# Optimization experiments

Measured on AMD Instinct MI355X. Metric: run time of the kernel, lower is better.

## Reference

```python
import jax
jax.config.update("jax_enable_x64", True)
import jax.numpy as jnp
import numpy as np

SAMPLE_RATE = 44100
HOP = 512
B, N_MELS, T = 8, 128, 2048
L = T * HOP  # 1,048,576 samples


def _lerp_up(x, out_len):
    # torch F.interpolate(mode='linear', align_corners=True): [B,C,Tin]->[B,C,out_len]
    t_in = x.shape[-1]
    pos = jnp.arange(out_len, dtype=jnp.float64) * ((t_in - 1) / (out_len - 1))
    i0 = jnp.floor(pos).astype(jnp.int32)
    i1 = jnp.minimum(i0 + 1, t_in - 1)
    w = (pos - i0).astype(x.dtype)
    return x[..., i0] * (1 - w) + x[..., i1] * w


def _conv1d(x, w, b, pad):
    y = jax.lax.conv_general_dilated(x, w, (1,), [(pad, pad)],
                                     dimension_numbers=("NCH", "OIH", "NCH"))
    return y + b[None, :, None]


def setup_inputs() -> dict:
    key = jax.random.key(0)
    ks = jax.random.split(key, 9)
    mel_frames = jax.random.normal(ks[0], (B, N_MELS, T), dtype=jnp.float32)
    # realistic f0: 80..380 Hz
    f0_frames = 80.0 + 300.0 * jax.random.uniform(ks[1], (B, T), dtype=jnp.float32)
    noise = jax.random.normal(ks[2], (B, L), dtype=jnp.float32)
    w1 = jax.random.normal(ks[3], (128, N_MELS, 7), dtype=jnp.float32) * 0.05
    b1 = jnp.zeros((128,), jnp.float32)
    w2 = jax.random.normal(ks[4], (128, 128, 3), dtype=jnp.float32) * 0.05
    b2 = jnp.zeros((128,), jnp.float32)
    w3 = jax.random.normal(ks[5], (2, 128, 3), dtype=jnp.float32) * 0.05
    b3 = jnp.zeros((2,), jnp.float32)
    return {"mel_frames": mel_frames, "f0_frames": f0_frames, "noise": noise,
            "w1": w1, "b1": b1, "w2": w2, "b2": b2, "w3": w3, "b3": b3}


def reference(mel_frames, f0_frames, noise, w1, b1, w2, b2, w3, b3):
    # --- comb source ---
    f0 = _lerp_up(f0_frames[:, None, :], L)  # [B,1,L]
    phase = jnp.cumsum(f0.astype(jnp.float64) / SAMPLE_RATE, axis=-1)
    phase = phase - jnp.round(phase)
    phase = phase.astype(f0.dtype)
    combtooth = jnp.sinc(SAMPLE_RATE * phase / (f0 + 1e-8))[:, 0, :]  # [B,L]
    # --- magnitude network ---
    h = jax.nn.leaky_relu(_conv1d(mel_frames, w1, b1, 3), 0.2)
    h = jax.nn.leaky_relu(_conv1d(h, w2, b2, 1), 0.2)
    mags = jnp.clip(_conv1d(h, w3, b3, 1), 0.0, 1.0)  # [B,2,T]
    mags = _lerp_up(mags, L)  # [B,2,L]
    noise_sig = jnp.clip(noise * mags[:, 0, :], -1.0, 1.0)
    comb_sig = jnp.clip(combtooth * mags[:, 1, :], -1.0, 1.0)
    signal = jnp.clip(noise_sig + comb_sig, -1.0, 1.0)
    return (signal[:, None, :], (comb_sig[:, None, :], noise_sig[:, None, :]))
```

## Files before the change

kernel.cpp:

```cpp
#include <hip/hip_runtime.h>
#include <math.h>

#define BATCH 8
#define NMEL 128
#define TT 2048
#define LL 1048576
#define NCHUNK 128
#define CHUNK 8192

static constexpr double RATIO = 2047.0 / 1048575.0;
static constexpr double INV_SR = 1.0 / 44100.0;

__device__ __forceinline__ float f0_at(const float* __restrict__ row, int n) {
    double pos = (double)n * RATIO;
    double fp = floor(pos);
    int i0 = (int)fp;
    int i1 = i0 + 1; if (i1 > TT - 1) i1 = TT - 1;
    float w = (float)(pos - fp);
    return row[i0] * (1.0f - w) + row[i1] * w;
}

__global__ __launch_bounds__(256) void wtrans_kernel(
    const float* __restrict__ w1, const float* __restrict__ w2,
    float* __restrict__ w1t, float* __restrict__ w2t)
{
    int i = blockIdx.x * 256 + threadIdx.x;
    if (i < 896 * 128) {
        int m = i >> 7, co = i & 127;
        w1t[i] = w1[co * 896 + m];
    }
    if (i < 384 * 128) {
        int m = i >> 7, co = i & 127;
        w2t[i] = w2[co * 384 + m];
    }
}

#define XSTR 48
#define HSTR 44
__global__ __launch_bounds__(256, 2) void fused_conv(
    const float* __restrict__ mel,
    const float* __restrict__ w1t,
    const float* __restrict__ b1,
    const float* __restrict__ w2t,
    const float* __restrict__ b2,
    const float* __restrict__ w3,
    const float* __restrict__ b3,
    float* __restrict__ mags)
{
    __shared__ float Xs[NMEL * XSTR];
    __shared__ float H1[NMEL * HSTR];
    __shared__ float H2[NMEL * HSTR];
    __shared__ float red[2][4][32];

    int b  = blockIdx.x >> 6;
    int t0 = (blockIdx.x & 63) * 32;
    int tid = threadIdx.x;
    const float* melb = mel + (size_t)b * NMEL * TT;

    #pragma unroll
    for (int it = 0; it < 6; ++it) {
        int idx = tid + it * 256;
        int ci = idx / 12, q = idx - ci * 12;
        int t = t0 - 8 + q * 4;
        float4 v = make_float4(0.f, 0.f, 0.f, 0.f);
        if (t >= 0 && t + 3 < TT) v = *(const float4*)(melb + ci * TT + t);
        *(float4*)(&Xs[ci * XSTR + q * 4]) = v;
    }
    if (tid < 128) { H1[tid * HSTR + 0] = 0.f; H1[tid * HSTR + 41] = 0.f; }
    __syncthreads();

    int cog = tid >> 3;
    int tg  = tid & 7;
    int xbase = 1 + tg * 5;

    {
        float acc[4][5];
        #pragma unroll
        for (int j = 0; j < 4; ++j) {
            float bj = b1[cog * 4 + j];
            #pragma unroll
            for (int i = 0; i < 5; ++i) acc[j][i] = bj;
        }
        for (int ci = 0; ci < NMEL; ++ci) {
            float xv[11];
            #pragma unroll
            for (int i = 0; i < 11; ++i) xv[i] = Xs[ci * XSTR + xbase + i];
            const float* wr = w1t + (size_t)(ci * 7) * 128 + cog * 4;
            #pragma unroll
            for (int k = 0; k < 7; ++k) {
                float4 w4 = *(const float4*)(wr + k * 128);
                float wv[4] = {w4.x, w4.y, w4.z, w4.w};
                #pragma unroll
                for (int j = 0; j < 4; ++j)
                    #pragma unroll
                    for (int i = 0; i < 5; ++i)
                        acc[j][i] = fmaf(wv[j], xv[i + k], acc[j][i]);
            }
        }
        #pragma unroll
        for (int j = 0; j < 4; ++j)
            #pragma unroll
            for (int i = 0; i < 5; ++i) {
                int t = t0 - 4 + tg * 5 + i;
                float v = acc[j][i];
                v = v > 0.0f ? v : 0.2f * v;
                if (t < 0 || t >= TT) v = 0.0f;
                H1[(cog * 4 + j) * HSTR + 1 + tg * 5 + i] = v;
            }
    }
    __syncthreads();

    {
        float acc[4][5];
        #pragma unroll
        for (int j = 0; j < 4; ++j) {
            float bj = b2[cog * 4 + j];
            #pragma unroll
            for (int i = 0; i < 5; ++i) acc[j][i] = bj;
        }
        int hbase = tg * 5;
        for (int ci = 0; ci < NMEL; ++ci) {
            float xv[7];
            #pragma unroll
            for (int i = 0; i < 7; ++i) xv[i] = H1[ci * HSTR + hbase + i];
            const float* wr = w2t + (size_t)(ci * 3) * 128 + cog * 4;
            #pragma unroll
            for (int k = 0; k < 3; ++k) {
                float4 w4 = *(const float4*)(wr + k * 128);
                float wv[4] = {w4.x, w4.y, w4.z, w4.w};
                #pragma unroll
                for (int j = 0; j < 4; ++j)
                    #pragma unroll
                    for (int i = 0; i < 5; ++i)
                        acc[j][i] = fmaf(wv[j], xv[i + k], acc[j][i]);
            }
        }
        #pragma unroll
        for (int j = 0; j < 4; ++j)
            #pragma unroll
            for (int i = 0; i < 5; ++i) {
                int t = t0 - 4 + tg * 5 + i;
                float v = acc[j][i];
                v = v > 0.0f ? v : 0.2f * v;
                if (t < 0 || t >= TT) v = 0.0f;
                H2[(cog * 4 + j) * HSTR + tg * 5 + i] = v;
            }
    }
    __syncthreads();

    {
        int o   = tid >> 7;
        int cig = (tid >> 5) & 3;
        int tt  = tid & 31;
        float a = 0.0f;
        for (int cl = 0; cl < 32; ++cl) {
            int ci = cig * 32 + cl;
            #pragma unroll
            for (int k = 0; k < 3; ++k)
                a = fmaf(w3[o * 384 + ci * 3 + k], H2[ci * HSTR + tt + 3 + k], a);
        }
        red[o][cig][tt] = a;
    }
    __syncthreads();
    if (tid < 64) {
        int o = tid >> 5, tt = tid & 31;
        float s = b3[o] + red[o][0][tt] + red[o][1][tt] + red[o][2][tt] + red[o][3][tt];
        s = fminf(fmaxf(s, 0.0f), 1.0f);
        mags[((size_t)b * 2 + o) * TT + t0 + tt] = s;
    }
}

__global__ __launch_bounds__(256) void chunksum_kernel(
    const float* __restrict__ f0f, double* __restrict__ sums)
{
    int b = blockIdx.x >> 7;
    int c = blockIdx.x & (NCHUNK - 1);
    const float* row = f0f + b * TT;
    int tid = threadIdx.x;
    int start = c * CHUNK + tid * 32;
    double s = 0.0;
    #pragma unroll
    for (int i = 0; i < 32; ++i)
        s += (double)f0_at(row, start + i) * INV_SR;
    __shared__ double red[256];
    red[tid] = s;
    __syncthreads();
    for (int off = 128; off > 0; off >>= 1) {
        if (tid < off) red[tid] += red[tid + off];
        __syncthreads();
    }
    if (tid == 0) sums[blockIdx.x] = red[0];
}

__global__ void scanoff_kernel(const double* __restrict__ sums, double* __restrict__ offs)
{
    int b = threadIdx.x;
    if (b < BATCH) {
        double run = 0.0;
        for (int c = 0; c < NCHUNK; ++c) {
            offs[b * NCHUNK + c] = run;
            run += sums[b * NCHUNK + c];
        }
    }
}

__device__ __forceinline__ int swz(int idx) { return idx ^ ((idx >> 5) & 31); }

__global__ __launch_bounds__(256) void final_kernel(
    const float* __restrict__ f0f,
    const float* __restrict__ noise,
    const float* __restrict__ mags,
    const double* __restrict__ offs,
    float* __restrict__ out)
{
    int b = blockIdx.x >> 7;
    int c = blockIdx.x & (NCHUNK - 1);
    const float* row = f0f + b * TT;
    int tid = threadIdx.x;
    __shared__ float fracs[CHUNK];
    __shared__ double red[256];

    int chunkBase = c * CHUNK;
    int start = chunkBase + tid * 32;

    float f0v[32];
    double s = 0.0;
    #pragma unroll
    for (int i = 0; i < 32; ++i) {
        f0v[i] = f0_at(row, start + i);
        s += (double)f0v[i] * INV_SR;
    }
    red[tid] = s;
    __syncthreads();
    for (int off = 1; off < 256; off <<= 1) {
        double v = (tid >= off) ? red[tid - off] : 0.0;
        __syncthreads();
        red[tid] += v;
        __syncthreads();
    }
    double run = offs[b * NCHUNK + c] + red[tid] - s;

    #pragma unroll
    for (int i = 0; i < 32; ++i) {
        run += (double)f0v[i] * INV_SR;
        double fr = run - rint(run);
        fracs[swz(tid * 32 + i)] = (float)fr;
    }
    __syncthreads();

    const size_t BL = (size_t)BATCH * LL;
    const size_t outBase = (size_t)b * LL;
    const float* m0row = mags + (size_t)b * 2 * TT;
    const float* m1row = m0row + TT;

    #pragma unroll 4
    for (int i = 0; i < 32; ++i) {
        int idx = i * 256 + tid;
        int n = chunkBase + idx;
        double pos = (double)n * RATIO;
        double fp = floor(pos);
        int i0 = (int)fp;
        int i1 = i0 + 1; if (i1 > TT - 1) i1 = TT - 1;
        float w = (float)(pos - fp);
        float f0 = row[i0] * (1.0f - w) + row[i1] * w;
        float m0 = m0row[i0] * (1.0f - w) + m0row[i1] * w;
        float m1 = m1row[i0] * (1.0f - w) + m1row[i1] * w;
        float ph = fracs[swz(idx)];
        float x = 44100.0f * ph / (f0 + 1e-8f);
        float px = 3.14159265358979323f * x;
        float comb = (x == 0.0f) ? 1.0f : (sinf(px) / px);
        float nz = noise[outBase + n];
        float ns = fminf(fmaxf(nz * m0, -1.0f), 1.0f);
        float cs = fminf(fmaxf(comb * m1, -1.0f), 1.0f);
        float sig = fminf(fmaxf(ns + cs, -1.0f), 1.0f);
        out[outBase + n]          = sig;
        out[BL + outBase + n]     = cs;
        out[2 * BL + outBase + n] = ns;
    }
}

extern "C" void kernel_launch(void* const* d_in, const int* in_sizes, int n_in,
                              void* d_out, int out_size, void* d_ws, size_t ws_size,
                              hipStream_t stream) {
    const float* mel   = (const float*)d_in[0];
    const float* f0f   = (const float*)d_in[1];
    const float* noise = (const float*)d_in[2];
    const float* w1    = (const float*)d_in[3];
    const float* b1    = (const float*)d_in[4];
    const float* w2    = (const float*)d_in[5];
    const float* b2    = (const float*)d_in[6];
    const float* w3    = (const float*)d_in[7];
    const float* b3    = (const float*)d_in[8];
    float* out = (float*)d_out;

    float* w1t  = (float*)d_ws;
    float* w2t  = w1t + 896 * 128;
    float* mags = w2t + 384 * 128;
    double* sums = (double*)(mags + BATCH * 2 * TT);
    double* offs = sums + BATCH * NCHUNK;

    wtrans_kernel<<<(896 * 128 + 255) / 256, 256, 0, stream>>>(w1, w2, w1t, w2t);
    fused_conv<<<BATCH * 64, 256, 0, stream>>>(mel, w1t, b1, w2t, b2, w3, b3, mags);
    chunksum_kernel<<<BATCH * NCHUNK, 256, 0, stream>>>(f0f, sums);
    scanoff_kernel<<<1, 64, 0, stream>>>(sums, offs);
    final_kernel<<<BATCH * NCHUNK, 256, 0, stream>>>(f0f, noise, mags, offs, out);
}
```

Baseline: 283.3 us.

## Merge conv and chunk-sum kernels, vectorize final kernel with fast sin

Folds the chunk-sum pass into the conv kernel as extra blocks so the two run in one launch and can overlap. Shared memory is reused between the conv stages, with an added barrier, to allow more blocks per CU. The final kernel now uses a wavefront shuffle scan instead of a shared-memory Hillis-Steele scan and processes four samples per thread with float4 loads and stores. It also computes sinc with hardware v_sin and reciprocal approximations, trading some accuracy for fewer instructions.

```diff
diff --git a/kernel.cpp b/kernel.cpp
--- a/kernel.cpp
+++ b/kernel.cpp
@@ -37,7 +37,7 @@
 
 #define XSTR 48
 #define HSTR 44
-__global__ __launch_bounds__(256, 2) void fused_conv(
+__global__ __launch_bounds__(256, 3) void conv_chunk_kernel(
     const float* __restrict__ mel,
     const float* __restrict__ w1t,
     const float* __restrict__ b1,
@@ -45,16 +45,41 @@
     const float* __restrict__ b2,
     const float* __restrict__ w3,
     const float* __restrict__ b3,
-    float* __restrict__ mags)
+    float* __restrict__ mags,
+    const float* __restrict__ f0f,
+    double* __restrict__ sums)
 {
-    __shared__ float Xs[NMEL * XSTR];
-    __shared__ float H1[NMEL * HSTR];
-    __shared__ float H2[NMEL * HSTR];
-    __shared__ float red[2][4][32];
+    __shared__ __align__(16) float smem[NMEL * XSTR + NMEL * HSTR + 256];
+    int tid = threadIdx.x;
+
+    if (blockIdx.x >= 512) {
+        int cb = blockIdx.x - 512;
+        int b = cb >> 7;
+        int c = cb & (NCHUNK - 1);
+        const float* row = f0f + b * TT;
+        int start = c * CHUNK + tid * 32;
+        double s = 0.0;
+        #pragma unroll
+        for (int i = 0; i < 32; ++i)
+            s += (double)f0_at(row, start + i) * INV_SR;
+        double* dred = (double*)smem;
+        dred[tid] = s;
+        __syncthreads();
+        for (int off = 128; off > 0; off >>= 1) {
+            if (tid < off) dred[tid] += dred[tid + off];
+            __syncthreads();
+        }
+        if (tid == 0) sums[cb] = dred[0];
+        return;
+    }
+
+    float* Xs  = smem;
+    float* H1  = smem + NMEL * XSTR;
+    float* H2  = smem;
+    float* red = smem + NMEL * XSTR + NMEL * HSTR;
 
     int b  = blockIdx.x >> 6;
     int t0 = (blockIdx.x & 63) * 32;
-    int tid = threadIdx.x;
     const float* melb = mel + (size_t)b * NMEL * TT;
 
     #pragma unroll
@@ -81,6 +106,7 @@
             #pragma unroll
             for (int i = 0; i < 5; ++i) acc[j][i] = bj;
         }
+        #pragma unroll 2
         for (int ci = 0; ci < NMEL; ++ci) {
             float xv[11];
             #pragma unroll
@@ -97,6 +123,7 @@
                         acc[j][i] = fmaf(wv[j], xv[i + k], acc[j][i]);
             }
         }
+        __syncthreads();
         #pragma unroll
         for (int j = 0; j < 4; ++j)
             #pragma unroll
@@ -119,6 +146,7 @@
             for (int i = 0; i < 5; ++i) acc[j][i] = bj;
         }
         int hbase = tg * 5;
+        #pragma unroll 2
         for (int ci = 0; ci < NMEL; ++ci) {
             float xv[7];
             #pragma unroll
@@ -159,37 +187,16 @@
             for (int k = 0; k < 3; ++k)
                 a = fmaf(w3[o * 384 + ci * 3 + k], H2[ci * HSTR + tt + 3 + k], a);
         }
-        red[o][cig][tt] = a;
+        red[(o * 4 + cig) * 32 + tt] = a;
     }
     __syncthreads();
     if (tid < 64) {
         int o = tid >> 5, tt = tid & 31;
-        float s = b3[o] + red[o][0][tt] + red[o][1][tt] + red[o][2][tt] + red[o][3][tt];
+        float s = b3[o] + red[(o * 4 + 0) * 32 + tt] + red[(o * 4 + 1) * 32 + tt]
+                        + red[(o * 4 + 2) * 32 + tt] + red[(o * 4 + 3) * 32 + tt];
         s = fminf(fmaxf(s, 0.0f), 1.0f);
         mags[((size_t)b * 2 + o) * TT + t0 + tt] = s;
     }
-}
-
-__global__ __launch_bounds__(256) void chunksum_kernel(
-    const float* __restrict__ f0f, double* __restrict__ sums)
-{
-    int b = blockIdx.x >> 7;
-    int c = blockIdx.x & (NCHUNK - 1);
-    const float* row = f0f + b * TT;
-    int tid = threadIdx.x;
-    int start = c * CHUNK + tid * 32;
-    double s = 0.0;
-    #pragma unroll
-    for (int i = 0; i < 32; ++i)
-        s += (double)f0_at(row, start + i) * INV_SR;
-    __shared__ double red[256];
-    red[tid] = s;
-    __syncthreads();
-    for (int off = 128; off > 0; off >>= 1) {
-        if (tid < off) red[tid] += red[tid + off];
-        __syncthreads();
-    }
-    if (tid == 0) sums[blockIdx.x] = red[0];
 }
 
 __global__ void scanoff_kernel(const double* __restrict__ sums, double* __restrict__ offs)
@@ -204,9 +211,9 @@
     }
 }
 
-__device__ __forceinline__ int swz(int idx) { return idx ^ ((idx >> 5) & 31); }
-
-__global__ __launch_bounds__(256) void final_kernel(
+__device__ __forceinline__ int swz4(int g) { return g ^ ((g >> 3) & 7); }
+
+__global__ __launch_bounds__(256, 4) void final_kernel(
     const float* __restrict__ f0f,
     const float* __restrict__ noise,
     const float* __restrict__ mags,
@@ -217,8 +224,9 @@
     int c = blockIdx.x & (NCHUNK - 1);
     const float* row = f0f + b * TT;
     int tid = threadIdx.x;
-    __shared__ float fracs[CHUNK];
-    __shared__ double red[256];
+    int lane = tid & 63, wid = tid >> 6;
+    __shared__ float4 fracsV[CHUNK / 4];
+    __shared__ double wsum[4];
 
     int chunkBase = c * CHUNK;
     int start = chunkBase + tid * 32;
@@ -230,21 +238,25 @@
         f0v[i] = f0_at(row, start + i);
         s += (double)f0v[i] * INV_SR;
     }
-    red[tid] = s;
-    __syncthreads();
-    for (int off = 1; off < 256; off <<= 1) {
-        double v = (tid >= off) ? red[tid - off] : 0.0;
-        __syncthreads();
-        red[tid] += v;
-        __syncthreads();
-    }
-    double run = offs[b * NCHUNK + c] + red[tid] - s;
-
+    double sinc_ = s;
+    #pragma unroll
+    for (int off = 1; off < 64; off <<= 1) {
+        double v = __shfl_up(sinc_, (unsigned)off, 64);
+        if (lane >= off) sinc_ += v;
+    }
+    if (lane == 63) wsum[wid] = sinc_;
+    __syncthreads();
+    double run = offs[b * NCHUNK + c] + (sinc_ - s);
+    for (int w = 0; w < wid; ++w) run += wsum[w];
+
+    float fb[4];
     #pragma unroll
     for (int i = 0; i < 32; ++i) {
         run += (double)f0v[i] * INV_SR;
         double fr = run - rint(run);
-        fracs[swz(tid * 32 + i)] = (float)fr;
+        fb[i & 3] = (float)fr;
+        if ((i & 3) == 3)
+            fracsV[swz4(tid * 8 + (i >> 2))] = make_float4(fb[0], fb[1], fb[2], fb[3]);
     }
     __syncthreads();
 
@@ -253,29 +265,55 @@
     const float* m0row = mags + (size_t)b * 2 * TT;
     const float* m1row = m0row + TT;
 
-    #pragma unroll 4
-    for (int i = 0; i < 32; ++i) {
-        int idx = i * 256 + tid;
-        int n = chunkBase + idx;
-        double pos = (double)n * RATIO;
-        double fp = floor(pos);
-        int i0 = (int)fp;
-        int i1 = i0 + 1; if (i1 > TT - 1) i1 = TT - 1;
-        float w = (float)(pos - fp);
-        float f0 = row[i0] * (1.0f - w) + row[i1] * w;
-        float m0 = m0row[i0] * (1.0f - w) + m0row[i1] * w;
-        float m1 = m1row[i0] * (1.0f - w) + m1row[i1] * w;
-        float ph = fracs[swz(idx)];
-        float x = 44100.0f * ph / (f0 + 1e-8f);
-        float px = 3.14159265358979323f * x;
-        float comb = (x == 0.0f) ? 1.0f : (sinf(px) / px);
-        float nz = noise[outBase + n];
-        float ns = fminf(fmaxf(nz * m0, -1.0f), 1.0f);
-        float cs = fminf(fmaxf(comb * m1, -1.0f), 1.0f);
-        float sig = fminf(fmaxf(ns + cs, -1.0f), 1.0f);
-        out[outBase + n]          = sig;
-        out[BL + outBase + n]     = cs;
-        out[2 * BL + outBase + n] = ns;
+    #pragma unroll 2
+    for (int g = 0; g < 8; ++g) {
+        int G = g * 256 + tid;
+        int n0 = chunkBase + G * 4;
+        float4 fr4 = fracsV[swz4(G)];
+        const float* frp = (const float*)&fr4;
+        float4 nz4 = *(const float4*)(noise + outBase + n0);
+        const float* nzp = (const float*)&nz4;
+
+        double pos0 = (double)n0 * RATIO;
+        int i0a = (int)floor(pos0);
+        int ib = i0a + 1 > TT - 1 ? TT - 1 : i0a + 1;
+        int ic = i0a + 2 > TT - 1 ? TT - 1 : i0a + 2;
+        float f0a = row[i0a],   f0b = row[ib],   f0c = row[ic];
+        float m0a = m0row[i0a], m0b = m0row[ib], m0c = m0row[ic];
+        float m1a = m1row[i0a], m1b = m1row[ib], m1c = m1row[ic];
+
+        float so[4], co_[4], no_[4];
+        #pragma unroll
+        for (int j = 0; j < 4; ++j) {
+            double pos = (double)(n0 + j) * RATIO;
+            double fp = floor(pos);
+            int i0 = (int)fp;
+            float w = (float)(pos - fp);
+            bool hi = i0 > i0a;
+            float xa = hi ? f0b : f0a, xb = hi ? f0c : f0b;
+            float f0 = xa * (1.0f - w) + xb * w;
+            float ya = hi ? m0b : m0a, yb = hi ? m0c : m0b;
+            float m0 = ya * (1.0f - w) + yb * w;
+            float za = hi ? m1b : m1a, zb = hi ? m1c : m1b;
+            float m1 = za * (1.0f - w) + zb * w;
+
+            float ph = frp[j];
+            float x  = 44100.0f * ph * __builtin_amdgcn_rcpf(f0 + 1e-8f);
+            float px = 3.14159265358979323f * x;
+            float rr = 0.5f * x;
+            float rf = rr - rintf(rr);
+            float sn;
+            asm("v_sin_f32 %0, %1" : "=v"(sn) : "v"(rf));
+            float comb = (x == 0.0f) ? 1.0f : sn * __builtin_amdgcn_rcpf(px);
+
+            float ns = fminf(fmaxf(nzp[j] * m0, -1.0f), 1.0f);
+            float cs = fminf(fmaxf(comb * m1, -1.0f), 1.0f);
+            so[j] = fminf(fmaxf(ns + cs, -1.0f), 1.0f);
+            co_[j] = cs; no_[j] = ns;
+        }
+        *(float4*)(out + outBase + n0)          = make_float4(so[0], so[1], so[2], so[3]);
+        *(float4*)(out + BL + outBase + n0)     = make_float4(co_[0], co_[1], co_[2], co_[3]);
+        *(float4*)(out + 2 * BL + outBase + n0) = make_float4(no_[0], no_[1], no_[2], no_[3]);
     }
 }
 
@@ -300,8 +338,8 @@
     double* offs = sums + BATCH * NCHUNK;
 
     wtrans_kernel<<<(896 * 128 + 255) / 256, 256, 0, stream>>>(w1, w2, w1t, w2t);
-    fused_conv<<<BATCH * 64, 256, 0, stream>>>(mel, w1t, b1, w2t, b2, w3, b3, mags);
-    chunksum_kernel<<<BATCH * NCHUNK, 256, 0, stream>>>(f0f, sums);
+    conv_chunk_kernel<<<512 + BATCH * NCHUNK, 256, 0, stream>>>(
+        mel, w1t, b1, w2t, b2, w3, b3, mags, f0f, sums);
     scanoff_kernel<<<1, 64, 0, stream>>>(sums, offs);
     final_kernel<<<BATCH * NCHUNK, 256, 0, stream>>>(f0f, noise, mags, offs, out);
 }
```

After: 254.8 us. 1.11x faster.
